# Optimization experiments

Hardware: AMD Instinct MI355X
Metric: run time of the kernel (lower is better)

## Reference

```python
import jax, jax.numpy as jnp
import numpy as np
import math

NUM_HEADS = 16
NUM_KV_HEADS = 4
HEAD_DIM = 128
ROPE_THETA = 10000.0


def _rope(x, cos, sin):
    # x: [b, h, s, d]; cos/sin: [1, 1, s, d//2]
    half = x.shape[-1] // 2
    x1, x2 = x[..., :half], x[..., half:]
    return jnp.concatenate([x1 * cos - x2 * sin, x2 * cos + x1 * sin], axis=-1)


def setup_inputs() -> dict:
    key = jax.random.key(0)
    ks = jax.random.split(key, 5)
    B, S, H = 2, 2048, 2048
    scale_qk = (2.0 / (H + H)) ** 0.5
    scale_kv = (2.0 / (H + NUM_KV_HEADS * HEAD_DIM)) ** 0.5
    return {
        "hidden_states": jax.random.normal(ks[0], (B, S, H), jnp.float32),
        "Wq": jax.random.normal(ks[1], (NUM_HEADS * HEAD_DIM, H), jnp.float32) * scale_qk,
        "Wk": jax.random.normal(ks[2], (NUM_KV_HEADS * HEAD_DIM, H), jnp.float32) * scale_kv,
        "Wv": jax.random.normal(ks[3], (NUM_KV_HEADS * HEAD_DIM, H), jnp.float32) * scale_kv,
        "Wo": jax.random.normal(ks[4], (NUM_HEADS * HEAD_DIM, H), jnp.float32) * scale_qk,
    }


def reference(hidden_states, Wq, Wk, Wv, Wo):
    B, S, H = hidden_states.shape
    hd = HEAD_DIM

    q = (hidden_states @ Wq.T).reshape(B, S, NUM_HEADS, hd).transpose(0, 2, 1, 3)
    k = (hidden_states @ Wk.T).reshape(B, S, NUM_KV_HEADS, hd).transpose(0, 2, 1, 3)
    v = (hidden_states @ Wv.T).reshape(B, S, NUM_KV_HEADS, hd).transpose(0, 2, 1, 3)

    # RoPE (half-split variant, as in module)
    inv_freq = 1.0 / (ROPE_THETA ** (jnp.arange(0, hd, 2, dtype=jnp.float32) / hd))
    pos = jnp.arange(S, dtype=jnp.float32)
    freqs = pos[:, None] * inv_freq[None, :]           # [S, hd//2]
    cos = jnp.cos(freqs)[None, None]                   # [1,1,S,hd//2]
    sin = jnp.sin(freqs)[None, None]
    q = _rope(q, cos, sin)
    k = _rope(k, cos, sin)

    # GQA: repeat kv heads (repeat_interleave semantics)
    n_rep = NUM_HEADS // NUM_KV_HEADS
    k = jnp.repeat(k, n_rep, axis=1)
    v = jnp.repeat(v, n_rep, axis=1)

    scores = jnp.einsum("bhqd,bhkd->bhqk", q, k) / math.sqrt(hd)
    attn = jax.nn.softmax(scores, axis=-1)
    out = jnp.einsum("bhqk,bhkd->bhqd", attn, v)
    out = out.transpose(0, 2, 1, 3).reshape(B, S, NUM_HEADS * hd)
    return out @ Wo.T
```

## Files before the change

### kernel.cpp

```cpp
#include <hip/hip_runtime.h>
#include <cstdint>
#include <cstddef>

typedef __bf16 bf16x8 __attribute__((ext_vector_type(8)));
typedef __bf16 bf16x4 __attribute__((ext_vector_type(4)));
typedef float  f32x4  __attribute__((ext_vector_type(4)));

__device__ __forceinline__ void gload_lds16(const void* g, void* l) {
    __builtin_amdgcn_global_load_lds(
        (const __attribute__((address_space(1))) void*)g,
        (__attribute__((address_space(3))) void*)l, 16, 0, 0);
}

#define VM6B asm volatile("s_waitcnt vmcnt(6) lgkmcnt(0)\ns_barrier" ::: "memory")
#define VM4B asm volatile("s_waitcnt vmcnt(4) lgkmcnt(0)\ns_barrier" ::: "memory")
#define VM0B asm volatile("s_waitcnt vmcnt(0) lgkmcnt(0)\ns_barrier" ::: "memory")
#define BARO asm volatile("s_barrier" ::: "memory")
#define WAITB4 asm volatile("s_waitcnt vmcnt(4) lgkmcnt(0)\ns_barrier" ::: "memory")
#define WAITB0 asm volatile("s_waitcnt vmcnt(0) lgkmcnt(0)\ns_barrier" ::: "memory")

#define SEQ 2048
#define NH 16
#define NKV 4
#define HD 128

__global__ __launch_bounds__(256) void cvt_all(const float* __restrict__ hs,
                                               const float* __restrict__ wq,
                                               const float* __restrict__ wk,
                                               const float* __restrict__ wv,
                                               const float* __restrict__ wo,
                                               __bf16* __restrict__ hB,
                                               __bf16* __restrict__ WqkB,
                                               __bf16* __restrict__ WvB,
                                               __bf16* __restrict__ WoB) {
    int bid = blockIdx.x;
    const float* in; __bf16* out; int base;
    if (bid < 8192)        { in = hs; out = hB;                   base = bid; }
    else if (bid < 12288)  { in = wq; out = WqkB;                 base = bid - 8192; }
    else if (bid < 13312)  { in = wk; out = WqkB + 2048 * 2048;   base = bid - 12288; }
    else if (bid < 14336)  { in = wv; out = WvB;                  base = bid - 13312; }
    else                   { in = wo; out = WoB;                  base = bid - 14336; }
    int i = base * 256 + threadIdx.x;
    float4 v = ((const float4*)in)[i];
    bf16x4 o = { (__bf16)v.x, (__bf16)v.y, (__bf16)v.z, (__bf16)v.w };
    ((bf16x4*)out)[i] = o;
}

__device__ __forceinline__ void stage_half(const __bf16* __restrict__ M,
                                           char* dbuf, int bmn, int k0, int half,
                                           int wave, int lane) {
    char* hb = dbuf + (half & 1) * 32768 + (half >> 1) * 16384;
    int kbase = k0 + (half >> 1) * 32;
#pragma unroll
    for (int g = 0; g < 2; ++g) {
        int c = wave * 2 + g;
        int row = (c & 3) * 64 + lane;
        int ks = c >> 2;
        gload_lds16(M + (size_t)(bmn + row) * 2048 + kbase + ks * 8, hb + c * 1024);
    }
}

template <int KS, int MH>
__device__ __forceinline__ void phase_mfma(const __bf16* bA, const __bf16* bB,
                                           int quad, int l16, int wr128, int colbase,
                                           bf16x8 (&bq)[4], f32x4 acc[8][4]) {
    bf16x8 af[4];
#pragma unroll
    for (int ii = 0; ii < 4; ++ii)
        af[ii] = *(const bf16x8*)(bA + (KS * 4 + quad) * 2048 +
                                  (wr128 + (MH * 4 + ii) * 16 + l16) * 8);
    if (MH == 0) {
#pragma unroll
        for (int j = 0; j < 4; ++j)
            bq[j] = *(const bf16x8*)(bB + (KS * 4 + quad) * 2048 +
                                     (colbase + (j & 1) * 16 + (j >> 1) * 64 + l16) * 8);
    }
    __builtin_amdgcn_s_setprio(1);
#pragma unroll
    for (int ii = 0; ii < 4; ++ii)
#pragma unroll
        for (int j = 0; j < 4; ++j)
            acc[MH * 4 + ii][j] = __builtin_amdgcn_mfma_f32_16x16x32_bf16(
                af[ii], bq[j], acc[MH * 4 + ii][j], 0, 0, 0);
    __builtin_amdgcn_s_setprio(0);
}

__device__ __forceinline__ void gemm_core(const __bf16* __restrict__ A,
                                          const __bf16* __restrict__ B,
                                          char* lds, int bm, int bn,
                                          int wave, int lane, int quad, int l16,
                                          int wr128, int colbase, f32x4 acc[8][4]) {
    const int NT = 32;
    stage_half(A, lds, bm, 0, 0, wave, lane);
    stage_half(B, lds, bn, 0, 1, wave, lane);
    stage_half(A, lds, bm, 0, 2, wave, lane);
    stage_half(B, lds, bn, 0, 3, wave, lane);
    int cur = 0;
    for (int t = 0; t < NT - 1; ++t) {
        const __bf16* bA = (const __bf16*)(lds + cur * 65536);
        const __bf16* bB = (const __bf16*)(lds + cur * 65536 + 32768);
        char* nb = lds + (cur ^ 1) * 65536;
        int k1 = (t + 1) * 64;
        bf16x8 bq[4];
        stage_half(A, nb, bm, k1, 0, wave, lane);
        VM6B;
        phase_mfma<0, 0>(bA, bB, quad, l16, wr128, colbase, bq, acc);
        stage_half(B, nb, bn, k1, 1, wave, lane);
        BARO;
        phase_mfma<0, 1>(bA, bB, quad, l16, wr128, colbase, bq, acc);
        stage_half(A, nb, bm, k1, 2, wave, lane);
        VM6B;
        phase_mfma<1, 0>(bA, bB, quad, l16, wr128, colbase, bq, acc);
        stage_half(B, nb, bn, k1, 3, wave, lane);
        BARO;
        phase_mfma<1, 1>(bA, bB, quad, l16, wr128, colbase, bq, acc);
        cur ^= 1;
    }
    {
        const __bf16* bA = (const __bf16*)(lds + cur * 65536);
        const __bf16* bB = (const __bf16*)(lds + cur * 65536 + 32768);
        bf16x8 bq[4];
        VM4B;
        phase_mfma<0, 0>(bA, bB, quad, l16, wr128, colbase, bq, acc);
        phase_mfma<0, 1>(bA, bB, quad, l16, wr128, colbase, bq, acc);
        VM0B;
        phase_mfma<1, 0>(bA, bB, quad, l16, wr128, colbase, bq, acc);
        phase_mfma<1, 1>(bA, bB, quad, l16, wr128, colbase, bq, acc);
    }
}

__global__ __launch_bounds__(512, 2) void qkv_gemm(const __bf16* __restrict__ hB,
                                                   const __bf16* __restrict__ Wqk,
                                                   const __bf16* __restrict__ Wv,
                                                   __bf16* __restrict__ Qr,
                                                   __bf16* __restrict__ Kr,
                                                   __bf16* __restrict__ VT) {
    __shared__ __align__(16) char lds[2 * 65536];
    const int tid = threadIdx.x;
    const int wave = tid >> 6, lane = tid & 63;
    const int quad = lane >> 4, l16 = lane & 15;
    const int wr = wave >> 2, wc = wave & 3;
    int wg = blockIdx.y * 16 + blockIdx.x;
    wg = (wg & 7) * 24 + (wg >> 3);
    const int x = wg & 15, y = wg >> 4;
    const bool isVT = (y >= 10);
    const bool isQ = (y < 8);

    const __bf16* Amat = isVT ? Wv : hB;
    const __bf16* Bmat = isVT ? hB : (isQ ? Wqk : Wqk + 2048 * 2048);
    const int bm = isVT ? (y - 10) * 256 : x * 256;
    const int bn = isVT ? x * 256 : (isQ ? y * 256 : (y - 8) * 256);

    const int wr128 = wr * 128;
    const int colbase = (wc >> 1) * 128 + (wc & 1) * 32;

    f32x4 acc[8][4] = {};
    gemm_core(Amat, Bmat, lds, bm, bn, wave, lane, quad, l16, wr128, colbase, acc);

    if (isVT) {
#pragma unroll
        for (int i = 0; i < 8; ++i)
#pragma unroll
            for (int j = 0; j < 4; ++j) {
                int row = bm + wr128 + i * 16 + quad * 4;
                int col = bn + colbase + (j & 1) * 16 + (j >> 1) * 64 + l16;
#pragma unroll
                for (int r = 0; r < 4; ++r)
                    VT[(size_t)(row + r) * 4096 + col] = (__bf16)acc[i][j][r];
            }
    } else {
        __bf16* outp = isQ ? Qr : Kr;
        const float sc = isQ ? 0.08838834764831845f : 1.0f;
        const int nh = isQ ? NH : NKV;
        const int hh = (isQ ? y * 2 : (y - 8) * 2) + (wc >> 1);
#pragma unroll
        for (int j2 = 0; j2 < 2; ++j2) {
            int d = (wc & 1) * 32 + j2 * 16 + l16;
            float inv = exp2f(-(float)d * 0.2076205059304601f);
#pragma unroll
            for (int i = 0; i < 8; ++i)
#pragma unroll
                for (int r = 0; r < 4; ++r) {
                    int m = bm + wr128 + i * 16 + quad * 4 + r;
                    int s = m & (SEQ - 1), b = m >> 11;
                    float f = (float)s * inv;
                    float c = __cosf(f) * sc, sn = __sinf(f) * sc;
                    float x1 = acc[i][j2][r], x2 = acc[i][j2 + 2][r];
                    size_t rb = ((size_t)(b * nh + hh) * SEQ + s) * HD;
                    outp[rb + d]      = (__bf16)(x1 * c - x2 * sn);
                    outp[rb + d + 64] = (__bf16)(x2 * c + x1 * sn);
                }
        }
    }
}

__global__ __launch_bounds__(512, 1) void gemm_bt_f32(const __bf16* __restrict__ A,
                                                      const __bf16* __restrict__ W,
                                                      float* __restrict__ C) {
    __shared__ __align__(16) char lds[3 * 49152];
    const int tid = threadIdx.x;
    const int wave = tid >> 6, lane = tid & 63;
    const int quad = lane >> 4, l16 = lane & 15;
    const int wr = wave >> 2, wc = wave & 3;
    int wg = blockIdx.y * 32 + blockIdx.x;
    wg = (wg & 7) * 32 + (wg >> 3);
    const int bm = (wg & 31) * 128, bn = (wg >> 5) * 256;

    f32x4 acc[4][4] = {};

    auto stageT = [&](int sb, int k0) {
        char* dst = lds + sb * 49152;
#pragma unroll
        for (int tt = 0; tt < 6; ++tt) {
            int c = wave * 6 + tt;
            if (c < 16) {
                int row = ((c & 1) << 6) + lane;
                gload_lds16(A + (size_t)(bm + row) * 2048 + k0 + (c >> 1) * 8,
                            dst + c * 1024);
            } else {
                int vc = c - 16;
                int row = ((vc & 3) << 6) + lane;
                gload_lds16(W + (size_t)(bn + row) * 2048 + k0 + (vc >> 2) * 8,
                            dst + 16384 + vc * 1024);
            }
        }
    };

    auto computeT = [&](int cb2) {
        const __bf16* bA = (const __bf16*)(lds + cb2 * 49152);
        const __bf16* bB = bA + 8192;
#pragma unroll
        for (int ks = 0; ks < 2; ++ks) {
            bf16x8 af[4], bq[4];
#pragma unroll
            for (int i = 0; i < 4; ++i)
                af[i] = *(const bf16x8*)(bA + (ks * 4 + quad) * 1024 +
                                         (wr * 64 + i * 16 + l16) * 8);
#pragma unroll
            for (int j = 0; j < 4; ++j)
                bq[j] = *(const bf16x8*)(bB + (ks * 4 + quad) * 2048 +
                                         (wc * 64 + j * 16 + l16) * 8);
            __builtin_amdgcn_s_setprio(1);
#pragma unroll
            for (int i = 0; i < 4; ++i)
#pragma unroll
                for (int j = 0; j < 4; ++j)
                    acc[i][j] = __builtin_amdgcn_mfma_f32_16x16x32_bf16(
                        af[i], bq[j], acc[i][j], 0, 0, 0);
            __builtin_amdgcn_s_setprio(0);
        }
    };

    stageT(0, 0);
    stageT(1, 64);
    int cb = 0;
    for (int t = 0; t < 31; ++t) {
        VM6B;
        if (t < 30) {
            int sb = cb + 2; if (sb >= 3) sb -= 3;
            stageT(sb, (t + 2) * 64);
        }
        computeT(cb);
        if (++cb == 3) cb = 0;
    }
    VM0B;
    computeT(cb);

#pragma unroll
    for (int i = 0; i < 4; ++i)
#pragma unroll
        for (int j = 0; j < 4; ++j) {
            int row = bm + wr * 64 + i * 16 + quad * 4;
            int col = bn + wc * 64 + j * 16 + l16;
#pragma unroll
            for (int r = 0; r < 4; ++r)
                C[(size_t)(row + r) * 2048 + col] = acc[i][j][r];
        }
}

__global__ __launch_bounds__(256, 2) void attn_kernel(const __bf16* __restrict__ Q,
                                                      const __bf16* __restrict__ Kr,
                                                      const __bf16* __restrict__ VT,
                                                      __bf16* __restrict__ AO) {
    __shared__ __align__(16) char ring[3 * 16384];
    __shared__ __align__(16) __bf16 Pb[4][32][40];

    const int tid = threadIdx.x;
    const int wave = tid >> 6, lane = tid & 63;
    const int quad = lane >> 4, l16 = lane & 15;
    int wg = (blockIdx.z * 16 + blockIdx.y) * 16 + blockIdx.x;
    wg = (wg & 7) * 64 + (wg >> 3);
    const int x = wg & 15, h = (wg >> 4) & 15, b = wg >> 8;
    const int kv = h >> 2;
    const int qbase = x * 128 + wave * 32;

    bf16x8 qf[2][4];
#pragma unroll
    for (int qs = 0; qs < 2; ++qs) {
        const __bf16* Qp =
            Q + ((size_t)(b * NH + h) * SEQ + qbase + qs * 16 + l16) * HD + quad * 8;
#pragma unroll
        for (int kq = 0; kq < 4; ++kq) qf[qs][kq] = *(const bf16x8*)(Qp + kq * 32);
    }

    const __bf16* Kp = Kr + (size_t)(b * NKV + kv) * SEQ * HD;
    const __bf16* Vp = VT + (size_t)(kv * HD) * (2 * SEQ) + b * SEQ;

    f32x4 oacc[2][8] = {};
    float lpart[2] = {0.f, 0.f};

    auto stage = [&](int sb, int k0) {
        char* dst = ring + sb * 16384;
#pragma unroll
        for (int tt = 0; tt < 4; ++tt) {
            int c = wave * 4 + tt;
            if (c < 8) {
                gload_lds16(Kp + (size_t)(k0 + (lane & 31)) * HD +
                                (2 * c + (lane >> 5)) * 8,
                            dst + c * 1024);
            } else {
                int vc = c - 8;
                gload_lds16(Vp + (size_t)(((vc & 1) << 6) + lane) * (2 * SEQ) + k0 +
                                (vc >> 1) * 8,
                            dst + 8192 + vc * 1024);
            }
        }
    };

    auto compute = [&](int cb) {
        const __bf16* kt = (const __bf16*)(ring + cb * 16384);
        const __bf16* vt = kt + 4096;
#pragma unroll
        for (int mt = 0; mt < 2; ++mt) {
            f32x4 s0 = {0.f, 0.f, 0.f, 0.f}, s1 = {0.f, 0.f, 0.f, 0.f};
#pragma unroll
            for (int kq = 0; kq < 4; ++kq) {
                bf16x8 ka = *(const bf16x8*)(kt + (kq * 4 + quad) * 256 +
                                             (mt * 16 + l16) * 8);
                s0 = __builtin_amdgcn_mfma_f32_16x16x32_bf16(ka, qf[0][kq], s0, 0, 0, 0);
                s1 = __builtin_amdgcn_mfma_f32_16x16x32_bf16(ka, qf[1][kq], s1, 0, 0, 0);
            }
            bf16x4 pk0, pk1;
#pragma unroll
            for (int r = 0; r < 4; ++r) {
                float p0 = __expf(s0[r]);
                float p1 = __expf(s1[r]);
                lpart[0] += p0; lpart[1] += p1;
                pk0[r] = (__bf16)p0; pk1[r] = (__bf16)p1;
            }
            *(bf16x4*)&Pb[wave][l16][mt * 16 + quad * 4] = pk0;
            *(bf16x4*)&Pb[wave][16 + l16][mt * 16 + quad * 4] = pk1;
        }
        bf16x8 pb0 = *(const bf16x8*)&Pb[wave][l16][quad * 8];
        bf16x8 pb1 = *(const bf16x8*)&Pb[wave][16 + l16][quad * 8];
#pragma unroll
        for (int mt = 0; mt < 8; ++mt) {
            bf16x8 va = *(const bf16x8*)(vt + quad * 1024 + (mt * 16 + l16) * 8);
            oacc[0][mt] = __builtin_amdgcn_mfma_f32_16x16x32_bf16(
                va, pb0, oacc[0][mt], 0, 0, 0);
            oacc[1][mt] = __builtin_amdgcn_mfma_f32_16x16x32_bf16(
                va, pb1, oacc[1][mt], 0, 0, 0);
        }
    };

    stage(0, 0);
    stage(1, 32);
    int cb = 0;
    for (int t = 0; t < 63; ++t) {
        WAITB4;
        if (t < 62) {
            int sb = cb + 2; if (sb >= 3) sb -= 3;
            stage(sb, (t + 2) * 32);
        }
        compute(cb);
        if (++cb == 3) cb = 0;
    }
    WAITB0;
    compute(cb);

#pragma unroll
    for (int qs = 0; qs < 2; ++qs) {
        lpart[qs] += __shfl_xor(lpart[qs], 16);
        lpart[qs] += __shfl_xor(lpart[qs], 32);
        float inv = 1.f / lpart[qs];
        int q = qbase + qs * 16 + l16;
#pragma unroll
        for (int mt = 0; mt < 8; ++mt) {
            bf16x4 ov;
#pragma unroll
            for (int r = 0; r < 4; ++r) ov[r] = (__bf16)(oacc[qs][mt][r] * inv);
            *(bf16x4*)(AO + ((size_t)(b * SEQ + q)) * (NH * HD) + h * HD +
                       mt * 16 + quad * 4) = ov;
        }
    }
}

extern "C" void kernel_launch(void* const* d_in, const int* in_sizes, int n_in,
                              void* d_out, int out_size, void* d_ws, size_t ws_size,
                              hipStream_t stream) {
    const float* hs = (const float*)d_in[0];
    const float* Wq = (const float*)d_in[1];
    const float* Wk = (const float*)d_in[2];
    const float* Wv = (const float*)d_in[3];
    const float* Wo = (const float*)d_in[4];
    float* out = (float*)d_out;
    char* ws = (char*)d_ws;

    __bf16* Qr   = (__bf16*)(ws + 0);
    __bf16* Kr   = (__bf16*)(ws + 16777216);
    __bf16* VT   = (__bf16*)(ws + 20971520);
    __bf16* WoB  = (__bf16*)(ws + 25165824);
    __bf16* hB   = (__bf16*)(ws + 33554432);
    __bf16* WqkB = (__bf16*)(ws + 50331648);
    __bf16* WvB  = (__bf16*)(ws + 60817408);
    __bf16* AO   = (__bf16*)(ws + 33554432);

    cvt_all<<<18432, 256, 0, stream>>>(hs, Wq, Wk, Wv, Wo, hB, WqkB, WvB, WoB);

    qkv_gemm<<<dim3(16, 12), 512, 0, stream>>>(hB, WqkB, WvB, Qr, Kr, VT);

    attn_kernel<<<dim3(16, 16, 2), 256, 0, stream>>>(Qr, Kr, VT, AO);

    gemm_bt_f32<<<dim3(32, 8), 512, 0, stream>>>(AO, WoB, out);
}
```

Baseline: 334.4 us.

## Transpose QK projection GEMM, vectorize RoPE stores, stage output GEMM through LDS

The Q/K projection now computes W·h^T, so each accumulator column is one token and head dims run along rows. The RoPE epilogue can then write contiguous bf16x4 vectors per token instead of scattered scalar stores. The output GEMM stages its fp32 tile through padded LDS and writes coalesced float4 rows. The softmax exponent switches to exp2 with log2(e) folded into the Q scale, which saves a multiply per score. This changes the operand roles in gemm_core and relies on the LDS being reusable after the main loop.

```diff
diff --git a/kernel.cpp b/kernel.cpp
--- a/kernel.cpp
+++ b/kernel.cpp
@@ -144,18 +144,16 @@
     wg = (wg & 7) * 24 + (wg >> 3);
     const int x = wg & 15, y = wg >> 4;
     const bool isVT = (y >= 10);
-    const bool isQ = (y < 8);
-
-    const __bf16* Amat = isVT ? Wv : hB;
-    const __bf16* Bmat = isVT ? hB : (isQ ? Wqk : Wqk + 2048 * 2048);
-    const int bm = isVT ? (y - 10) * 256 : x * 256;
-    const int bn = isVT ? x * 256 : (isQ ? y * 256 : (y - 8) * 256);
+
+    const __bf16* Amat = isVT ? Wv : Wqk;
+    const int bm = (isVT ? (y - 10) : y) * 256;
+    const int bn = x * 256;
 
     const int wr128 = wr * 128;
     const int colbase = (wc >> 1) * 128 + (wc & 1) * 32;
 
     f32x4 acc[8][4] = {};
-    gemm_core(Amat, Bmat, lds, bm, bn, wave, lane, quad, l16, wr128, colbase, acc);
+    gemm_core(Amat, hB, lds, bm, bn, wave, lane, quad, l16, wr128, colbase, acc);
 
     if (isVT) {
 #pragma unroll
@@ -169,27 +167,38 @@
                     VT[(size_t)(row + r) * 4096 + col] = (__bf16)acc[i][j][r];
             }
     } else {
+        const bool isQ = (y < 8);
         __bf16* outp = isQ ? Qr : Kr;
-        const float sc = isQ ? 0.08838834764831845f : 1.0f;
+        const float sc = isQ ? 0.1275255128608411f : 1.0f;
         const int nh = isQ ? NH : NKV;
-        const int hh = (isQ ? y * 2 : (y - 8) * 2) + (wc >> 1);
-#pragma unroll
-        for (int j2 = 0; j2 < 2; ++j2) {
-            int d = (wc & 1) * 32 + j2 * 16 + l16;
-            float inv = exp2f(-(float)d * 0.2076205059304601f);
-#pragma unroll
-            for (int i = 0; i < 8; ++i)
+        const int hh = ((bm + wr128) >> 7) - (isQ ? 0 : 16);
+        float invt[4][4];
+#pragma unroll
+        for (int i = 0; i < 4; ++i)
+#pragma unroll
+            for (int r = 0; r < 4; ++r)
+                invt[i][r] = exp2f(-(float)(i * 16 + quad * 4 + r) *
+                                   0.2076205059304601f);
+#pragma unroll
+        for (int j = 0; j < 4; ++j) {
+            int scol = bn + colbase + (j & 1) * 16 + (j >> 1) * 64 + l16;
+            int b = scol >> 11, s = scol & (SEQ - 1);
+            __bf16* rowp = outp + ((size_t)(b * nh + hh) * SEQ + s) * HD;
+            float sf = (float)s;
+#pragma unroll
+            for (int i = 0; i < 4; ++i) {
+                bf16x4 o1, o2;
 #pragma unroll
                 for (int r = 0; r < 4; ++r) {
-                    int m = bm + wr128 + i * 16 + quad * 4 + r;
-                    int s = m & (SEQ - 1), b = m >> 11;
-                    float f = (float)s * inv;
+                    float f = sf * invt[i][r];
                     float c = __cosf(f) * sc, sn = __sinf(f) * sc;
-                    float x1 = acc[i][j2][r], x2 = acc[i][j2 + 2][r];
-                    size_t rb = ((size_t)(b * nh + hh) * SEQ + s) * HD;
-                    outp[rb + d]      = (__bf16)(x1 * c - x2 * sn);
-                    outp[rb + d + 64] = (__bf16)(x2 * c + x1 * sn);
+                    float x1 = acc[i][j][r], x2 = acc[i + 4][j][r];
+                    o1[r] = (__bf16)(x1 * c - x2 * sn);
+                    o2[r] = (__bf16)(x2 * c + x1 * sn);
                 }
+                *(bf16x4*)(rowp + i * 16 + quad * 4) = o1;
+                *(bf16x4*)(rowp + 64 + i * 16 + quad * 4) = o2;
+            }
         }
     }
 }
@@ -266,16 +275,27 @@
     VM0B;
     computeT(cb);
 
+    __syncthreads();
+    float* Cst = (float*)lds;
 #pragma unroll
     for (int i = 0; i < 4; ++i)
 #pragma unroll
         for (int j = 0; j < 4; ++j) {
-            int row = bm + wr * 64 + i * 16 + quad * 4;
-            int col = bn + wc * 64 + j * 16 + l16;
+            int row = wr * 64 + i * 16 + quad * 4;
+            int col = wc * 64 + j * 16 + l16;
 #pragma unroll
             for (int r = 0; r < 4; ++r)
-                C[(size_t)(row + r) * 2048 + col] = acc[i][j][r];
-        }
+                Cst[(row + r) * 260 + col] = acc[i][j][r];
+        }
+    __syncthreads();
+    {
+        int row = tid >> 2, colq = tid & 3;
+        const float* src = Cst + row * 260 + colq * 64;
+        float* dst = C + (size_t)(bm + row) * 2048 + bn + colq * 64;
+#pragma unroll
+        for (int c = 0; c < 16; ++c)
+            *(float4*)(dst + c * 4) = *(const float4*)(src + c * 4);
+    }
 }
 
 __global__ __launch_bounds__(256, 2) void attn_kernel(const __bf16* __restrict__ Q,
@@ -343,8 +363,8 @@
             bf16x4 pk0, pk1;
 #pragma unroll
             for (int r = 0; r < 4; ++r) {
-                float p0 = __expf(s0[r]);
-                float p1 = __expf(s1[r]);
+                float p0 = exp2f(s0[r]);
+                float p1 = exp2f(s1[r]);
                 lpart[0] += p0; lpart[1] += p1;
                 pk0[r] = (__bf16)p0; pk1[r] = (__bf16)p1;
             }
```

After: 373.3 us. +11.6%, slower.
